# Optimization experiments

Hardware: AMD Instinct MI355X
Metric: run time of the kernel (lower is better)

Reference implementation:

```python
import jax, jax.numpy as jnp
import numpy as np

T, B, W, L = 64, 32, 1024, 4  # time, batch, hidden(=input) width, layers


def setup_inputs() -> dict:
    key = jax.random.key(0)
    ks = jax.random.split(key, 5)
    x = jax.random.normal(ks[0], (T, B, W), dtype=jnp.float32)
    resets = jax.random.randint(ks[1], (T, B), 0, 2).astype(bool)
    c0 = jnp.zeros((L, B, W), dtype=jnp.float32)
    h0 = jnp.zeros((L, B, W), dtype=jnp.float32)
    # Per-layer LSTM params (flax LSTMCell gate order: i, f, g, o concatenated).
    scale = 1.0 / np.sqrt(W)
    Wx = jax.random.normal(ks[2], (L, W, 4 * W), dtype=jnp.float32) * scale
    Wh = jax.random.normal(ks[3], (L, W, 4 * W), dtype=jnp.float32) * scale
    b = jnp.zeros((L, 4 * W), dtype=jnp.float32)
    return {"x": x, "resets": resets, "c0": c0, "h0": h0,
            "Wx": Wx, "Wh": Wh, "b": b}


def _lstm_scan(x, resets, c0, h0, Wx, Wh, b):
    num_layers = Wx.shape[0]

    def step(carry, xt):
        cs, hs = carry                      # each [L, B, W]
        ins, reset = xt                     # [B, W], [B]
        mask = reset[None, :, None]
        cs = jnp.where(mask, 0.0, cs)
        hs = jnp.where(mask, 0.0, hs)
        y = ins
        new_cs, new_hs = [], []
        for l in range(num_layers):
            gates = y @ Wx[l] + hs[l] @ Wh[l] + b[l]   # [B, 4W]
            i, f, g, o = jnp.split(gates, 4, axis=-1)
            c = jax.nn.sigmoid(f) * cs[l] + jax.nn.sigmoid(i) * jnp.tanh(g)
            h = jax.nn.sigmoid(o) * jnp.tanh(c)
            y = h
            new_cs.append(c)
            new_hs.append(h)
        return (jnp.stack(new_cs), jnp.stack(new_hs)), y

    (cs_f, hs_f), ys = jax.lax.scan(step, (c0, h0), (x, resets))
    return ys, cs_f, hs_f


def reference(x, resets, c0, h0, Wx, Wh, b):
    # ys: [T, B, W] stacked top-layer outputs; final carry also returned.
    return _lstm_scan(x, resets, c0, h0, Wx, Wh, b)
```

## Files before the change

### kernel.cpp

```cpp
#include <hip/hip_runtime.h>
#include <stdint.h>


typedef unsigned short u16;
typedef unsigned int u32;
typedef __attribute__((ext_vector_type(8))) short short8;
typedef __attribute__((ext_vector_type(4))) float f32x4;

#define NT 64
#define NB 32
#define NW 1024
#define NLAY 4
#define G4 4096

#define HIST_OFF 0
#define FLAGS_OFF 17039360
#define RMASK_OFF 17104896
#define MODE_OFF 17113088

__device__ __forceinline__ float bf2f(u16 u) {
  union { u32 i; float f; } v; v.i = ((u32)u) << 16; return v.f;
}
__device__ __forceinline__ u16 f2bf(float f) {
  union { float f; u32 i; } v; v.f = f;
  u32 b = v.i;
  return (u16)((b + 0x7FFFu + ((b >> 16) & 1u)) >> 16);
}
__device__ __forceinline__ float sigmoidf_(float x) { return 1.f / (1.f + __expf(-x)); }
__device__ __forceinline__ float tanhfast(float x) {
  float cx = fminf(fmaxf(x, -15.f), 15.f);
  float e = __expf(2.f * cx);
  return (e - 1.f) / (e + 1.f);
}

__global__ void lstm_setup(const void* __restrict__ x, const void* __restrict__ resets,
                           int* __restrict__ modes, int* __restrict__ rmask,
                           int* __restrict__ flags) {
  __shared__ int votes_bf16, bad_int, bad_float;
  __shared__ int sm_rmode;
  int tid = threadIdx.x;
  if (tid == 0) { votes_bf16 = 0; bad_int = 0; bad_float = 0; }
  __syncthreads();

  {
    u32 w = ((const u32*)x)[tid];
    int e = (int)((w >> 7) & 0xFFu);
    if (e >= 100 && e <= 140) atomicAdd(&votes_bf16, 1);
  }
  if (tid < 128) {
    u32 r = ((const u32*)resets)[tid];
    if (r > 1u) atomicAdd(&bad_int, 1);
    if (r != 0u && r != 0x3F800000u) atomicAdd(&bad_float, 1);
  }
  __syncthreads();
  if (tid == 0) {
    int mbf = (votes_bf16 >= 192) ? 1 : 0;
    int rmode;
    if (bad_int == 0) rmode = 1;
    else if (bad_float == 0) rmode = 2;
    else rmode = 0;
    modes[0] = mbf;
    modes[1] = rmode;
    sm_rmode = rmode;
  }
  __syncthreads();
  int rmode = sm_rmode;
#pragma unroll
  for (int k = 0; k < 8; ++k) {
    int idx = tid * 8 + k;
    int val;
    if (rmode == 1) val = (((const int*)resets)[idx] != 0);
    else if (rmode == 2) val = (((const u32*)resets)[idx] != 0u);
    else val = (((const unsigned char*)resets)[idx] != 0);
    rmask[idx] = val;
  }
  for (int k = tid; k < NLAY * NT * 64; k += 256) flags[k] = 0;
}

template <bool BF16>
__global__ void lstm_prep(const void* __restrict__ h0, const int* __restrict__ modes,
                          u16* __restrict__ hist) {
  if ((modes[0] != 0) != BF16) return;
  int idx = blockIdx.x * 256 + threadIdx.x;
  int l = idx >> 15;
  int rem = idx & 32767;
  float hv;
  if (BF16) hv = bf2f(((const u16*)h0)[idx]);
  else      hv = ((const float*)h0)[idx];
  hist[(size_t)l * (65 * NB * NW) + rem] = f2bf(hv);
}

template <bool BF16>
__global__ __launch_bounds__(256, 1) void lstm_main(
    const void* __restrict__ xv, const void* __restrict__ Wxv,
    const void* __restrict__ Whv, const void* __restrict__ biasv,
    const void* __restrict__ c0v,
    void* __restrict__ outv, const int* __restrict__ modes,
    const int* __restrict__ rmask, u16* __restrict__ hist,
    int* __restrict__ flags) {
  if ((modes[0] != 0) != BF16) return;

  const int l = blockIdx.x >> 6;
  const int s = blockIdx.x & 63;
  const int hb = s * 16;
  const int tid = threadIdx.x;
  const int wave = tid >> 6;
  const int lane = tid & 63;
  const bool xpart = (wave < 2);
  const int krel = (wave & 1) * 512;
  const int lrow = lane & 15;
  const int lk8 = (lane >> 4) * 8;

  const int eb = tid >> 3;
  const int n0 = (tid & 7) * 2;
  const int emt = eb >> 4, er = eb & 15;

  __shared__ float red[4][2][4][16][17];

  short8 wfrag[4][16];
  {
    const size_t base = (size_t)l * NW * G4;
#pragma unroll
    for (int g = 0; g < 4; ++g) {
#pragma unroll
      for (int kt = 0; kt < 16; ++kt) {
        size_t off = base + (size_t)(krel + kt * 32 + lk8) * G4 + (size_t)(g * 1024 + hb + lrow);
        short8 v;
        if (BF16) {
          const u16* p = (xpart ? (const u16*)Wxv : (const u16*)Whv) + off;
#pragma unroll
          for (int j = 0; j < 8; ++j) v[j] = (short)p[(size_t)j * G4];
        } else {
          const float* p = (xpart ? (const float*)Wxv : (const float*)Whv) + off;
#pragma unroll
          for (int j = 0; j < 8; ++j) v[j] = (short)f2bf(p[(size_t)j * G4]);
        }
        wfrag[g][kt] = v;
      }
    }
  }

  float bias_r[4][2];
#pragma unroll
  for (int g = 0; g < 4; ++g)
#pragma unroll
    for (int j = 0; j < 2; ++j) {
      int bidx = l * G4 + g * 1024 + hb + n0 + j;
      bias_r[g][j] = BF16 ? bf2f(((const u16*)biasv)[bidx]) : ((const float*)biasv)[bidx];
    }

  float creg[2] = {0.f, 0.f};

  short8 z8;
#pragma unroll
  for (int j = 0; j < 8; ++j) z8[j] = 0;

#pragma unroll 1
  for (int t = 0; t < NT; ++t) {
    if (wave == 0 && l > 0) {
      const int* p = &flags[((l - 1) * NT + t) * 64 + lane];
      while (__hip_atomic_load(p, __ATOMIC_RELAXED, __HIP_MEMORY_SCOPE_AGENT) == 0)
        __builtin_amdgcn_s_sleep(1);
    }
    if (wave == 1 && t > 0) {
      const int* p = &flags[(l * NT + (t - 1)) * 64 + lane];
      while (__hip_atomic_load(p, __ATOMIC_RELAXED, __HIP_MEMORY_SCOPE_AGENT) == 0)
        __builtin_amdgcn_s_sleep(1);
    }
    __syncthreads();

    const u16* srcH = hist + ((size_t)l * 65 + t) * (NB * NW);
    const u16* srcY = hist + ((size_t)(l - 1) * 65 + (t + 1)) * (NB * NW);
    const u16* srcXb = (const u16*)xv + (size_t)t * NB * NW;
    const float* srcXf = (const float*)xv + (size_t)t * NB * NW;

    int rm0 = 0, rm1 = 0;
    if (!xpart) {
      rm0 = rmask[t * NB + lrow];
      rm1 = rmask[t * NB + 16 + lrow];
    }

    f32x4 acc[2][4];
    f32x4 zf = {0.f, 0.f, 0.f, 0.f};
#pragma unroll
    for (int mt = 0; mt < 2; ++mt)
#pragma unroll
      for (int g = 0; g < 4; ++g) acc[mt][g] = zf;

#pragma unroll
    for (int half = 0; half < 2; ++half) {
      short8 af[8][2];
#pragma unroll
      for (int q = 0; q < 8; ++q) {
        int kk = krel + (half * 8 + q) * 32 + lk8;
        short8 a0, a1;
        if (!xpart) {
          a0 = *(const short8*)(srcH + (size_t)lrow * NW + kk);
          a1 = *(const short8*)(srcH + (size_t)(lrow + 16) * NW + kk);
          if (rm0) a0 = z8;
          if (rm1) a1 = z8;
        } else if (l > 0) {
          a0 = *(const short8*)(srcY + (size_t)lrow * NW + kk);
          a1 = *(const short8*)(srcY + (size_t)(lrow + 16) * NW + kk);
        } else if (BF16) {
          a0 = *(const short8*)(srcXb + (size_t)lrow * NW + kk);
          a1 = *(const short8*)(srcXb + (size_t)(lrow + 16) * NW + kk);
        } else {
          const f32x4* p0 = (const f32x4*)(srcXf + (size_t)lrow * NW + kk);
          const f32x4* p1 = (const f32x4*)(srcXf + (size_t)(lrow + 16) * NW + kk);
          f32x4 x0a = p0[0], x0b = p0[1], x1a = p1[0], x1b = p1[1];
#pragma unroll
          for (int j = 0; j < 4; ++j) {
            a0[j] = (short)f2bf(x0a[j]);
            a0[j + 4] = (short)f2bf(x0b[j]);
            a1[j] = (short)f2bf(x1a[j]);
            a1[j + 4] = (short)f2bf(x1b[j]);
          }
        }
        af[q][0] = a0;
        af[q][1] = a1;
      }
#pragma unroll
      for (int q = 0; q < 8; ++q) {
        int kt = half * 8 + q;
#pragma unroll
        for (int g = 0; g < 4; ++g) {
          acc[0][g] = __builtin_amdgcn_mfma_f32_16x16x32_bf16(af[q][0], wfrag[g][kt], acc[0][g], 0, 0, 0);
          acc[1][g] = __builtin_amdgcn_mfma_f32_16x16x32_bf16(af[q][1], wfrag[g][kt], acc[1][g], 0, 0, 0);
        }
      }
    }

#pragma unroll
    for (int mt = 0; mt < 2; ++mt)
#pragma unroll
      for (int g = 0; g < 4; ++g)
#pragma unroll
        for (int r = 0; r < 4; ++r)
          red[wave][mt][g][(lane >> 4) * 4 + r][lrow] = acc[mt][g][r];
    __syncthreads();

    {
      int rm = rmask[t * NB + eb];
      float hn[2];
#pragma unroll
      for (int j = 0; j < 2; ++j) {
        int n = n0 + j;
        float gv[4];
#pragma unroll
        for (int g = 0; g < 4; ++g)
          gv[g] = red[0][emt][g][er][n] + red[1][emt][g][er][n] +
                  red[2][emt][g][er][n] + red[3][emt][g][er][n] + bias_r[g][j];
        float c_old = creg[j];
        if (t == 0) {
          int cidx = (l * NB + eb) * NW + hb + n;
          c_old = BF16 ? bf2f(((const u16*)c0v)[cidx]) : ((const float*)c0v)[cidx];
        }
        if (rm) c_old = 0.f;
        float ci = sigmoidf_(gv[0]);
        float cf = sigmoidf_(gv[1]);
        float cg = tanhfast(gv[2]);
        float co = sigmoidf_(gv[3]);
        float cn = cf * c_old + ci * cg;
        hn[j] = co * tanhfast(cn);
        creg[j] = cn;
      }
      u32 hp = (u32)f2bf(hn[0]) | ((u32)f2bf(hn[1]) << 16);
      size_t hoff = ((size_t)l * 65 + (t + 1)) * (NB * NW) + (size_t)eb * NW + hb + n0;
      __hip_atomic_store((u32*)(hist + hoff), hp, __ATOMIC_RELAXED, __HIP_MEMORY_SCOPE_AGENT);
      if (l == NLAY - 1) {
        size_t oy = ((size_t)t * NB + eb) * NW + hb + n0;
        if (BF16) ((u32*)outv)[oy >> 1] = hp;
        else { ((float*)outv)[oy] = hn[0]; ((float*)outv)[oy + 1] = hn[1]; }
      }
      if (t == NT - 1) {
        size_t oc = (size_t)NT * NB * NW + ((size_t)l * NB + eb) * NW + hb + n0;
        size_t oh = oc + (size_t)NLAY * NB * NW;
        if (BF16) {
          u32 cp = (u32)f2bf(creg[0]) | ((u32)f2bf(creg[1]) << 16);
          ((u32*)outv)[oc >> 1] = cp;
          ((u32*)outv)[oh >> 1] = hp;
        } else {
          ((float*)outv)[oc] = creg[0];
          ((float*)outv)[oc + 1] = creg[1];
          ((float*)outv)[oh] = hn[0];
          ((float*)outv)[oh + 1] = hn[1];
        }
      }
    }

    asm volatile("s_waitcnt vmcnt(0)" ::: "memory");
    __syncthreads();
    if (tid == 0)
      __hip_atomic_store(&flags[(l * NT + t) * 64 + s], 1, __ATOMIC_RELAXED,
                         __HIP_MEMORY_SCOPE_AGENT);
  }
}

extern "C" void kernel_launch(void* const* d_in, const int* in_sizes, int n_in,
                              void* d_out, int out_size, void* d_ws, size_t ws_size,
                              hipStream_t stream) {
  const void* x = d_in[0];
  const void* resets = d_in[1];
  const void* c0 = d_in[2];
  const void* h0 = d_in[3];
  const void* Wx = d_in[4];
  const void* Wh = d_in[5];
  const void* bias = d_in[6];

  char* ws = (char*)d_ws;
  u16* hist = (u16*)(ws + HIST_OFF);
  int* flags = (int*)(ws + FLAGS_OFF);
  int* rmask = (int*)(ws + RMASK_OFF);
  int* modes = (int*)(ws + MODE_OFF);

  lstm_setup<<<1, 256, 0, stream>>>(x, resets, modes, rmask, flags);
  lstm_prep<true><<<512, 256, 0, stream>>>(h0, modes, hist);
  lstm_prep<false><<<512, 256, 0, stream>>>(h0, modes, hist);
  lstm_main<true><<<256, 256, 0, stream>>>(x, Wx, Wh, bias, c0, d_out, modes, rmask, hist, flags);
  lstm_main<false><<<256, 256, 0, stream>>>(x, Wx, Wh, bias, c0, d_out, modes, rmask, hist, flags);
}
```

Baseline: 1.286 ms.

## Replace flag-based inter-block sync with poison-sentinel polling on hidden-state data

```diff
diff --git a/kernel.cpp b/kernel.cpp
--- a/kernel.cpp
+++ b/kernel.cpp
@@ -6,15 +6,16 @@
 typedef unsigned int u32;
 typedef __attribute__((ext_vector_type(8))) short short8;
 typedef __attribute__((ext_vector_type(4))) float f32x4;
+typedef __attribute__((ext_vector_type(4))) unsigned int u32x4;
 
 #define NT 64
 #define NB 32
 #define NW 1024
 #define NLAY 4
 #define G4 4096
+#define POISON 0xAAAAAAAAu
 
 #define HIST_OFF 0
-#define FLAGS_OFF 17039360
 #define RMASK_OFF 17104896
 #define MODE_OFF 17113088
 
@@ -32,16 +33,50 @@
   float e = __expf(2.f * cx);
   return (e - 1.f) / (e + 1.f);
 }
+union CastU { u32x4 u; short8 s; };
+__device__ __forceinline__ short8 as_s8(u32x4 v) { CastU c; c.u = v; return c.s; }
+__device__ __forceinline__ u32x4 as_u4(short8 v) { CastU c; c.s = v; return c.u; }
+
+__device__ __forceinline__ void poll_half(const u16* rowA, const u16* rowB, u32x4 r[16]) {
+  for (;;) {
+#pragma unroll
+    for (int q = 0; q < 8; ++q) {
+      asm volatile("global_load_dwordx4 %0, %1, off sc0 sc1" : "=v"(r[q]) : "v"(rowA + q * 32));
+      asm volatile("global_load_dwordx4 %0, %1, off sc0 sc1" : "=v"(r[8 + q]) : "v"(rowB + q * 32));
+    }
+    asm volatile("s_waitcnt vmcnt(0)"
+                 : "+v"(r[0]), "+v"(r[1]), "+v"(r[2]), "+v"(r[3]), "+v"(r[4]), "+v"(r[5]),
+                   "+v"(r[6]), "+v"(r[7]), "+v"(r[8]), "+v"(r[9]), "+v"(r[10]), "+v"(r[11]),
+                   "+v"(r[12]), "+v"(r[13]), "+v"(r[14]), "+v"(r[15])
+                 :
+                 : "memory");
+    bool ok = true;
+    const u16* probe = rowA;
+    bool have = false;
+#pragma unroll
+    for (int c = 0; c < 16; ++c) {
+      bool f = (r[c].x != POISON) && (r[c].y != POISON) && (r[c].z != POISON) && (r[c].w != POISON);
+      if (!f && !have) { probe = (c < 8) ? (rowA + c * 32) : (rowB + (c - 8) * 32); have = true; }
+      ok &= f;
+    }
+    if (ok) return;
+    for (;;) {
+      __builtin_amdgcn_s_sleep(4);
+      u32x4 v;
+      asm volatile("global_load_dwordx4 %0, %1, off sc0 sc1" : "=v"(v) : "v"(probe));
+      asm volatile("s_waitcnt vmcnt(0)" : "+v"(v) : : "memory");
+      if ((v.x != POISON) && (v.y != POISON) && (v.z != POISON) && (v.w != POISON)) break;
+    }
+  }
+}
 
 __global__ void lstm_setup(const void* __restrict__ x, const void* __restrict__ resets,
-                           int* __restrict__ modes, int* __restrict__ rmask,
-                           int* __restrict__ flags) {
+                           int* __restrict__ modes, int* __restrict__ rmask) {
   __shared__ int votes_bf16, bad_int, bad_float;
   __shared__ int sm_rmode;
   int tid = threadIdx.x;
   if (tid == 0) { votes_bf16 = 0; bad_int = 0; bad_float = 0; }
   __syncthreads();
-
   {
     u32 w = ((const u32*)x)[tid];
     int e = (int)((w >> 7) & 0xFFu);
@@ -74,7 +109,14 @@
     else val = (((const unsigned char*)resets)[idx] != 0);
     rmask[idx] = val;
   }
-  for (int k = tid; k < NLAY * NT * 64; k += 256) flags[k] = 0;
+}
+
+__global__ void lstm_poison(u32* __restrict__ hist32) {
+  int g = (blockIdx.x * 256 + threadIdx.x) * 4;
+  int l = g >> 20;
+  int r = g & 1048575;
+  u32x4 v = {POISON, POISON, POISON, POISON};
+  *(u32x4*)(hist32 + ((size_t)l * 65 + 1) * 16384 + r) = v;
 }
 
 template <bool BF16>
@@ -96,8 +138,7 @@
     const void* __restrict__ Whv, const void* __restrict__ biasv,
     const void* __restrict__ c0v,
     void* __restrict__ outv, const int* __restrict__ modes,
-    const int* __restrict__ rmask, u16* __restrict__ hist,
-    int* __restrict__ flags) {
+    const int* __restrict__ rmask, u16* __restrict__ hist) {
   if ((modes[0] != 0) != BF16) return;
 
   const int l = blockIdx.x >> 6;
@@ -151,24 +192,8 @@
 
   float creg[2] = {0.f, 0.f};
 
-  short8 z8;
-#pragma unroll
-  for (int j = 0; j < 8; ++j) z8[j] = 0;
-
 #pragma unroll 1
   for (int t = 0; t < NT; ++t) {
-    if (wave == 0 && l > 0) {
-      const int* p = &flags[((l - 1) * NT + t) * 64 + lane];
-      while (__hip_atomic_load(p, __ATOMIC_RELAXED, __HIP_MEMORY_SCOPE_AGENT) == 0)
-        __builtin_amdgcn_s_sleep(1);
-    }
-    if (wave == 1 && t > 0) {
-      const int* p = &flags[(l * NT + (t - 1)) * 64 + lane];
-      while (__hip_atomic_load(p, __ATOMIC_RELAXED, __HIP_MEMORY_SCOPE_AGENT) == 0)
-        __builtin_amdgcn_s_sleep(1);
-    }
-    __syncthreads();
-
     const u16* srcH = hist + ((size_t)l * 65 + t) * (NB * NW);
     const u16* srcY = hist + ((size_t)(l - 1) * 65 + (t + 1)) * (NB * NW);
     const u16* srcXb = (const u16*)xv + (size_t)t * NB * NW;
@@ -189,44 +214,54 @@
 
 #pragma unroll
     for (int half = 0; half < 2; ++half) {
-      short8 af[8][2];
+      u32x4 r[16];
+      const int kbase = krel + half * 256 + lk8;
+      if (xpart) {
+        if (l > 0) {
+          poll_half(srcY + (size_t)lrow * NW + kbase, srcY + (size_t)(lrow + 16) * NW + kbase, r);
+        } else if (BF16) {
+#pragma unroll
+          for (int q = 0; q < 8; ++q) {
+            r[q] = *(const u32x4*)(srcXb + (size_t)lrow * NW + kbase + q * 32);
+            r[8 + q] = *(const u32x4*)(srcXb + (size_t)(lrow + 16) * NW + kbase + q * 32);
+          }
+        } else {
+#pragma unroll
+          for (int q = 0; q < 8; ++q) {
+            const f32x4* p0 = (const f32x4*)(srcXf + (size_t)lrow * NW + kbase + q * 32);
+            const f32x4* p1 = (const f32x4*)(srcXf + (size_t)(lrow + 16) * NW + kbase + q * 32);
+            f32x4 x0a = p0[0], x0b = p0[1], x1a = p1[0], x1b = p1[1];
+            short8 a0, a1;
+#pragma unroll
+            for (int j = 0; j < 4; ++j) {
+              a0[j] = (short)f2bf(x0a[j]);
+              a0[j + 4] = (short)f2bf(x0b[j]);
+              a1[j] = (short)f2bf(x1a[j]);
+              a1[j + 4] = (short)f2bf(x1b[j]);
+            }
+            r[q] = as_u4(a0);
+            r[8 + q] = as_u4(a1);
+          }
+        }
+      } else {
+        poll_half(srcH + (size_t)lrow * NW + kbase, srcH + (size_t)(lrow + 16) * NW + kbase, r);
+        u32x4 z4 = {0u, 0u, 0u, 0u};
+        if (rm0) {
+#pragma unroll
+          for (int q = 0; q < 8; ++q) r[q] = z4;
+        }
+        if (rm1) {
+#pragma unroll
+          for (int q = 0; q < 8; ++q) r[8 + q] = z4;
+        }
+      }
 #pragma unroll
       for (int q = 0; q < 8; ++q) {
-        int kk = krel + (half * 8 + q) * 32 + lk8;
-        short8 a0, a1;
-        if (!xpart) {
-          a0 = *(const short8*)(srcH + (size_t)lrow * NW + kk);
-          a1 = *(const short8*)(srcH + (size_t)(lrow + 16) * NW + kk);
-          if (rm0) a0 = z8;
-          if (rm1) a1 = z8;
-        } else if (l > 0) {
-          a0 = *(const short8*)(srcY + (size_t)lrow * NW + kk);
-          a1 = *(const short8*)(srcY + (size_t)(lrow + 16) * NW + kk);
-        } else if (BF16) {
-          a0 = *(const short8*)(srcXb + (size_t)lrow * NW + kk);
-          a1 = *(const short8*)(srcXb + (size_t)(lrow + 16) * NW + kk);
-        } else {
-          const f32x4* p0 = (const f32x4*)(srcXf + (size_t)lrow * NW + kk);
-          const f32x4* p1 = (const f32x4*)(srcXf + (size_t)(lrow + 16) * NW + kk);
-          f32x4 x0a = p0[0], x0b = p0[1], x1a = p1[0], x1b = p1[1];
-#pragma unroll
-          for (int j = 0; j < 4; ++j) {
-            a0[j] = (short)f2bf(x0a[j]);
-            a0[j + 4] = (short)f2bf(x0b[j]);
-            a1[j] = (short)f2bf(x1a[j]);
-            a1[j + 4] = (short)f2bf(x1b[j]);
-          }
-        }
-        af[q][0] = a0;
-        af[q][1] = a1;
-      }
-#pragma unroll
-      for (int q = 0; q < 8; ++q) {
-        int kt = half * 8 + q;
+        const int kt = half * 8 + q;
 #pragma unroll
         for (int g = 0; g < 4; ++g) {
-          acc[0][g] = __builtin_amdgcn_mfma_f32_16x16x32_bf16(af[q][0], wfrag[g][kt], acc[0][g], 0, 0, 0);
-          acc[1][g] = __builtin_amdgcn_mfma_f32_16x16x32_bf16(af[q][1], wfrag[g][kt], acc[1][g], 0, 0, 0);
+          acc[0][g] = __builtin_amdgcn_mfma_f32_16x16x32_bf16(as_s8(r[q]), wfrag[g][kt], acc[0][g], 0, 0, 0);
+          acc[1][g] = __builtin_amdgcn_mfma_f32_16x16x32_bf16(as_s8(r[8 + q]), wfrag[g][kt], acc[1][g], 0, 0, 0);
         }
       }
     }
@@ -236,8 +271,8 @@
 #pragma unroll
       for (int g = 0; g < 4; ++g)
 #pragma unroll
-        for (int r = 0; r < 4; ++r)
-          red[wave][mt][g][(lane >> 4) * 4 + r][lrow] = acc[mt][g][r];
+        for (int r2 = 0; r2 < 4; ++r2)
+          red[wave][mt][g][(lane >> 4) * 4 + r2][lrow] = acc[mt][g][r2];
     __syncthreads();
 
     {
@@ -288,12 +323,7 @@
         }
       }
     }
-
-    asm volatile("s_waitcnt vmcnt(0)" ::: "memory");
     __syncthreads();
-    if (tid == 0)
-      __hip_atomic_store(&flags[(l * NT + t) * 64 + s], 1, __ATOMIC_RELAXED,
-                         __HIP_MEMORY_SCOPE_AGENT);
   }
 }
 
@@ -310,13 +340,13 @@
 
   char* ws = (char*)d_ws;
   u16* hist = (u16*)(ws + HIST_OFF);
-  int* flags = (int*)(ws + FLAGS_OFF);
   int* rmask = (int*)(ws + RMASK_OFF);
   int* modes = (int*)(ws + MODE_OFF);
 
-  lstm_setup<<<1, 256, 0, stream>>>(x, resets, modes, rmask, flags);
+  lstm_setup<<<1, 256, 0, stream>>>(x, resets, modes, rmask);
+  lstm_poison<<<4096, 256, 0, stream>>>((u32*)hist);
   lstm_prep<true><<<512, 256, 0, stream>>>(h0, modes, hist);
   lstm_prep<false><<<512, 256, 0, stream>>>(h0, modes, hist);
-  lstm_main<true><<<256, 256, 0, stream>>>(x, Wx, Wh, bias, c0, d_out, modes, rmask, hist, flags);
-  lstm_main<false><<<256, 256, 0, stream>>>(x, Wx, Wh, bias, c0, d_out, modes, rmask, hist, flags);
-}
+  lstm_main<true><<<256, 256, 0, stream>>>(x, Wx, Wh, bias, c0, d_out, modes, rmask, hist);
+  lstm_main<false><<<256, 256, 0, stream>>>(x, Wx, Wh, bias, c0, d_out, modes, rmask, hist);
+}
```

Result: faster. 1.038 ms (-19.3%).

## Tile hidden-state history, map layers to XCDs, and poll flags with uncached loads

Applied to the files above, without the earlier changes.

```diff
diff --git a/kernel.cpp b/kernel.cpp
--- a/kernel.cpp
+++ b/kernel.cpp
@@ -33,15 +33,21 @@
   return (e - 1.f) / (e + 1.f);
 }
 
+__device__ __forceinline__ u32 poll_load(const u32* p) {
+  u32 v;
+  asm volatile("global_load_dword %0, %1, off sc0 sc1" : "=v"(v) : "v"(p));
+  asm volatile("s_waitcnt vmcnt(0)" : "+v"(v) : : "memory");
+  return v;
+}
+
 __global__ void lstm_setup(const void* __restrict__ x, const void* __restrict__ resets,
                            int* __restrict__ modes, int* __restrict__ rmask,
-                           int* __restrict__ flags) {
+                           u32* __restrict__ flags) {
   __shared__ int votes_bf16, bad_int, bad_float;
   __shared__ int sm_rmode;
   int tid = threadIdx.x;
   if (tid == 0) { votes_bf16 = 0; bad_int = 0; bad_float = 0; }
   __syncthreads();
-
   {
     u32 w = ((const u32*)x)[tid];
     int e = (int)((w >> 7) & 0xFFu);
@@ -84,10 +90,13 @@
   int idx = blockIdx.x * 256 + threadIdx.x;
   int l = idx >> 15;
   int rem = idx & 32767;
+  int b = rem >> 10;
+  int w = rem & 1023;
   float hv;
   if (BF16) hv = bf2f(((const u16*)h0)[idx]);
   else      hv = ((const float*)h0)[idx];
-  hist[(size_t)l * (65 * NB * NW) + rem] = f2bf(hv);
+  size_t dst = (((size_t)l * 65 + 0) * 64 + (w >> 4)) * 512 + (size_t)b * 16 + (w & 15);
+  hist[dst] = f2bf(hv);
 }
 
 template <bool BF16>
@@ -97,12 +106,13 @@
     const void* __restrict__ c0v,
     void* __restrict__ outv, const int* __restrict__ modes,
     const int* __restrict__ rmask, u16* __restrict__ hist,
-    int* __restrict__ flags) {
+    u32* __restrict__ flags) {
   if ((modes[0] != 0) != BF16) return;
 
-  const int l = blockIdx.x >> 6;
-  const int s = blockIdx.x & 63;
-  const int hb = s * 16;
+  const int xcd = blockIdx.x & 7;
+  const int l = xcd & 3;
+  const int s2 = (blockIdx.x >> 3) + ((xcd >> 2) << 5);
+  const int hb = s2 * 16;
   const int tid = threadIdx.x;
   const int wave = tid >> 6;
   const int lane = tid & 63;
@@ -158,19 +168,17 @@
 #pragma unroll 1
   for (int t = 0; t < NT; ++t) {
     if (wave == 0 && l > 0) {
-      const int* p = &flags[((l - 1) * NT + t) * 64 + lane];
-      while (__hip_atomic_load(p, __ATOMIC_RELAXED, __HIP_MEMORY_SCOPE_AGENT) == 0)
-        __builtin_amdgcn_s_sleep(1);
-    }
-    if (wave == 1 && t > 0) {
-      const int* p = &flags[(l * NT + (t - 1)) * 64 + lane];
-      while (__hip_atomic_load(p, __ATOMIC_RELAXED, __HIP_MEMORY_SCOPE_AGENT) == 0)
-        __builtin_amdgcn_s_sleep(1);
+      const u32* fp = &flags[((size_t)(l - 1) * NT + t) * 64 + lane];
+      while (poll_load(fp) == 0) __builtin_amdgcn_s_sleep(1);
+    }
+    if (wave == 2 && t > 0) {
+      const u32* fp = &flags[((size_t)l * NT + (t - 1)) * 64 + lane];
+      while (poll_load(fp) == 0) __builtin_amdgcn_s_sleep(1);
     }
     __syncthreads();
 
-    const u16* srcH = hist + ((size_t)l * 65 + t) * (NB * NW);
-    const u16* srcY = hist + ((size_t)(l - 1) * 65 + (t + 1)) * (NB * NW);
+    const u16* srcH = hist + ((size_t)l * 65 + t) * (64 * 512);
+    const u16* srcY = hist + ((size_t)(l - 1) * 65 + (t + 1)) * (64 * 512);
     const u16* srcXb = (const u16*)xv + (size_t)t * NB * NW;
     const float* srcXf = (const float*)xv + (size_t)t * NB * NW;
 
@@ -192,22 +200,23 @@
       short8 af[8][2];
 #pragma unroll
       for (int q = 0; q < 8; ++q) {
-        int kk = krel + (half * 8 + q) * 32 + lk8;
+        int k = krel + (half * 8 + q) * 32 + lk8;
         short8 a0, a1;
-        if (!xpart) {
-          a0 = *(const short8*)(srcH + (size_t)lrow * NW + kk);
-          a1 = *(const short8*)(srcH + (size_t)(lrow + 16) * NW + kk);
-          if (rm0) a0 = z8;
-          if (rm1) a1 = z8;
-        } else if (l > 0) {
-          a0 = *(const short8*)(srcY + (size_t)lrow * NW + kk);
-          a1 = *(const short8*)(srcY + (size_t)(lrow + 16) * NW + kk);
+        if (!xpart || l > 0) {
+          const u16* src = xpart ? srcY : srcH;
+          const u16* pc = src + (size_t)(k >> 4) * 512 + (k & 15);
+          a0 = *(const short8*)(pc + lrow * 16);
+          a1 = *(const short8*)(pc + (lrow + 16) * 16);
+          if (!xpart) {
+            if (rm0) a0 = z8;
+            if (rm1) a1 = z8;
+          }
         } else if (BF16) {
-          a0 = *(const short8*)(srcXb + (size_t)lrow * NW + kk);
-          a1 = *(const short8*)(srcXb + (size_t)(lrow + 16) * NW + kk);
+          a0 = *(const short8*)(srcXb + (size_t)lrow * NW + k);
+          a1 = *(const short8*)(srcXb + (size_t)(lrow + 16) * NW + k);
         } else {
-          const f32x4* p0 = (const f32x4*)(srcXf + (size_t)lrow * NW + kk);
-          const f32x4* p1 = (const f32x4*)(srcXf + (size_t)(lrow + 16) * NW + kk);
+          const f32x4* p0 = (const f32x4*)(srcXf + (size_t)lrow * NW + k);
+          const f32x4* p1 = (const f32x4*)(srcXf + (size_t)(lrow + 16) * NW + k);
           f32x4 x0a = p0[0], x0b = p0[1], x1a = p1[0], x1b = p1[1];
 #pragma unroll
           for (int j = 0; j < 4; ++j) {
@@ -222,7 +231,7 @@
       }
 #pragma unroll
       for (int q = 0; q < 8; ++q) {
-        int kt = half * 8 + q;
+        const int kt = half * 8 + q;
 #pragma unroll
         for (int g = 0; g < 4; ++g) {
           acc[0][g] = __builtin_amdgcn_mfma_f32_16x16x32_bf16(af[q][0], wfrag[g][kt], acc[0][g], 0, 0, 0);
@@ -236,13 +245,13 @@
 #pragma unroll
       for (int g = 0; g < 4; ++g)
 #pragma unroll
-        for (int r = 0; r < 4; ++r)
-          red[wave][mt][g][(lane >> 4) * 4 + r][lrow] = acc[mt][g][r];
+        for (int r2 = 0; r2 < 4; ++r2)
+          red[wave][mt][g][(lane >> 4) * 4 + r2][lrow] = acc[mt][g][r2];
     __syncthreads();
 
+    float hn[2];
     {
       int rm = rmask[t * NB + eb];
-      float hn[2];
 #pragma unroll
       for (int j = 0; j < 2; ++j) {
         int n = n0 + j;
@@ -266,7 +275,7 @@
         creg[j] = cn;
       }
       u32 hp = (u32)f2bf(hn[0]) | ((u32)f2bf(hn[1]) << 16);
-      size_t hoff = ((size_t)l * 65 + (t + 1)) * (NB * NW) + (size_t)eb * NW + hb + n0;
+      size_t hoff = (((size_t)l * 65 + (t + 1)) * 64 + s2) * 512 + (size_t)eb * 16 + n0;
       __hip_atomic_store((u32*)(hist + hoff), hp, __ATOMIC_RELAXED, __HIP_MEMORY_SCOPE_AGENT);
       if (l == NLAY - 1) {
         size_t oy = ((size_t)t * NB + eb) * NW + hb + n0;
@@ -292,8 +301,8 @@
     asm volatile("s_waitcnt vmcnt(0)" ::: "memory");
     __syncthreads();
     if (tid == 0)
-      __hip_atomic_store(&flags[(l * NT + t) * 64 + s], 1, __ATOMIC_RELAXED,
-                         __HIP_MEMORY_SCOPE_AGENT);
+      __hip_atomic_store(&flags[((size_t)l * NT + t) * 64 + s2], 1u,
+                         __ATOMIC_RELAXED, __HIP_MEMORY_SCOPE_AGENT);
   }
 }
 
@@ -310,7 +319,7 @@
 
   char* ws = (char*)d_ws;
   u16* hist = (u16*)(ws + HIST_OFF);
-  int* flags = (int*)(ws + FLAGS_OFF);
+  u32* flags = (u32*)(ws + FLAGS_OFF);
   int* rmask = (int*)(ws + RMASK_OFF);
   int* modes = (int*)(ws + MODE_OFF);
 
```

Result: faster. 1.115 ms (-13.3%).
